# Kernel tuning notes

Hardware: AMD Instinct MI355X
Metric: run time of the kernel (lower is better)

The kernel has to match this reference:

```python
import jax, jax.numpy as jnp
import numpy as np

# Multi-res hash grid config (tiny-cuda-nn defaults matching input_ch=32 = 16 levels * 2 feats)
L = 16            # n_levels
F = 2             # n_features_per_level
T = 2 ** 19       # hashmap size per level
BASE_RES = 16
FINEST_RES = 512
_b = np.exp((np.log(FINEST_RES) - np.log(BASE_RES)) / (L - 1))
RES = np.floor(BASE_RES * (_b ** np.arange(L))).astype(np.float32)  # (L,)
PRIMES = jnp.array([1, 2654435761, 805459861], dtype=jnp.uint32)
# 8 binary corner offsets of a voxel
CORNERS = jnp.array([[(i >> d) & 1 for d in range(3)] for i in range(8)], dtype=jnp.uint32)  # (8,3)


def hash_encode(x, tables):
    """x: (N,3) in [0,1]; tables: (L, T, F). Returns (N, L*F)."""
    res = jnp.asarray(RES)                              # (L,)
    xs = x[None, :, :] * res[:, None, None]             # (L,N,3) scaled coords
    x0f = jnp.floor(xs)
    frac = xs - x0f                                     # (L,N,3)
    x0 = x0f.astype(jnp.uint32)
    corners = x0[:, :, None, :] + CORNERS[None, None]   # (L,N,8,3) uint32
    # spatial hash: xor of coord*prime, wraparound uint32 mul
    h = (corners[..., 0] * PRIMES[0]) ^ (corners[..., 1] * PRIMES[1]) ^ (corners[..., 2] * PRIMES[2])
    idx = (h % jnp.uint32(T)).astype(jnp.int32)         # (L,N,8)
    gidx = idx + (jnp.arange(L, dtype=jnp.int32) * T)[:, None, None]
    feats = tables.reshape(L * T, F)[gidx]              # (L,N,8,F) gather
    # trilinear weights per corner
    w = jnp.prod(jnp.where(CORNERS[None, None] == 1, frac[:, :, None, :], 1.0 - frac[:, :, None, :]), axis=-1)  # (L,N,8)
    out = jnp.einsum('lnc,lncf->lnf', w, feats)         # (L,N,F)
    return out.transpose(1, 0, 2).reshape(x.shape[0], L * F)


def setup_inputs() -> dict:
    key = jax.random.key(0)
    ks = jax.random.split(key, 16)
    N = 1048576
    W = 128
    pos_flat = jax.random.uniform(ks[0], (N, 3), dtype=jnp.float32)  # world pts in unit cube
    bbox_min = jnp.zeros((3,), dtype=jnp.float32)
    bbox_max = jnp.ones((3,), dtype=jnp.float32)
    tables = jax.random.uniform(ks[1], (L, T, F), dtype=jnp.float32, minval=-1e-4, maxval=1e-4)
    def lin(k, fan_in, fan_out):
        s = 1.0 / np.sqrt(fan_in)
        return jax.random.uniform(k, (fan_in, fan_out), dtype=jnp.float32, minval=-s, maxval=s)
    return {
        'pos_flat': pos_flat, 'bbox_min': bbox_min, 'bbox_max': bbox_max, 'tables': tables,
        'W0': lin(ks[2], L * F, W), 'b0': jnp.zeros((W,), jnp.float32),
        'W1': lin(ks[3], W, W), 'b1': jnp.zeros((W,), jnp.float32),
        'W2': lin(ks[4], W, W), 'b2': jnp.zeros((W,), jnp.float32),
        'W3': lin(ks[5], W, W), 'b3': jnp.zeros((W,), jnp.float32),
        'Wout': lin(ks[6], W, 4), 'bout': jnp.zeros((4,), jnp.float32),
    }


def reference(pos_flat, bbox_min, bbox_max, tables, W0, b0, W1, b1, W2, b2, W3, b3, Wout, bout):
    # normalize into canonical bbox [0,1]^3
    x = (pos_flat - bbox_min) / (bbox_max - bbox_min)
    h = hash_encode(x, tables)                # (N, 32)
    h = jax.nn.relu(h @ W0 + b0)
    h = jax.nn.relu(h @ W1 + b1)
    h = jax.nn.relu(h @ W2 + b2)
    h = jax.nn.relu(h @ W3 + b3)
    raws = h @ Wout + bout                    # (N, 4) rgb + density
    return raws
```

## Files before the change

kernel.cpp:

```cpp
#include <hip/hip_runtime.h>

typedef _Float16 half8 __attribute__((ext_vector_type(8)));
typedef _Float16 half4 __attribute__((ext_vector_type(4)));
typedef _Float16 half2 __attribute__((ext_vector_type(2)));
typedef float    f32x4 __attribute__((ext_vector_type(4)));
typedef float    f32x2 __attribute__((ext_vector_type(2)));
typedef unsigned u32x2 __attribute__((ext_vector_type(2)));
typedef unsigned u32x4 __attribute__((ext_vector_type(4)));

#define TMASK ((1u << 19) - 1u)
#define HSTRIDE 136
constexpr float SCALE = 65536.0f;
constexpr float INV_SCALE = 1.0f / 65536.0f;

__device__ __constant__ unsigned SC_TAB[8]   = {18, 22, 27, 34, 42, 52, 66, 82};
__device__ __constant__ unsigned SX4_TAB[8]  = {5, 6, 7, 9, 11, 13, 17, 21};
__device__ __constant__ unsigned DOFF16_TAB[8] = {0, 1620, 4524, 9627, 20031, 39435, 74587, 148639};
#define DSLOT_TOTAL 289843u

__global__ void prep_kernel(const float* __restrict__ W0, const float* __restrict__ W1,
                            const float* __restrict__ W2, const float* __restrict__ W3,
                            const float* __restrict__ Wm,
                            const float* __restrict__ b0, const float* __restrict__ b1,
                            const float* __restrict__ b2, const float* __restrict__ b3,
                            const float* __restrict__ bm,
                            _Float16* __restrict__ wsW, float* __restrict__ wsB,
                            const float* __restrict__ tabSrc, _Float16* __restrict__ tabF,
                            int tabBlocks)
{
    if ((int)blockIdx.x < tabBlocks) {
        size_t i = (size_t)blockIdx.x * 256 + threadIdx.x;
        f32x4 v = ((const f32x4*)tabSrc)[i];
        half4 o;
        o[0] = (_Float16)(v.x * SCALE);
        o[1] = (_Float16)(v.y * SCALE);
        o[2] = (_Float16)(v.z * SCALE);
        o[3] = (_Float16)(v.w * SCALE);
        ((half4*)tabF)[i] = o;
        return;
    }
    int gid = ((int)blockIdx.x - tabBlocks) * 256 + threadIdx.x;
    if (gid < 6912) {
        int tile = gid >> 6, lane = gid & 63;
        const float* W; int K, N, toff;
        if (tile < 8)        { W = W0; K = 32;  N = 128; toff = 0;   }
        else if (tile < 40)  { W = W1; K = 128; N = 128; toff = 8;   }
        else if (tile < 72)  { W = W2; K = 128; N = 128; toff = 40;  }
        else if (tile < 104) { W = W3; K = 128; N = 128; toff = 72;  }
        else                 { W = Wm; K = 128; N = 4;   toff = 104; }
        int tt = tile - toff;
        int KT = K >> 5;
        int nt = tt / KT, kt = tt - nt * KT;
        int n = nt * 16 + (lane & 15);
        int kbase = kt * 32 + (lane >> 4) * 8;
        half8 v;
        #pragma unroll
        for (int j = 0; j < 8; j++) {
            int k = kbase + j;
            float w = (n < N) ? W[k * N + n] : 0.0f;
            v[j] = (_Float16)w;
        }
        *(half8*)(wsW + (size_t)gid * 8) = v;
    } else if (gid < 6912 + 528) {
        int i = gid - 6912;
        float v;
        if (i < 512) {
            int layer = i >> 7, n = i & 127;
            const float* b = (layer == 0) ? b0 : (layer == 1) ? b1 : (layer == 2) ? b2 : b3;
            v = b[n] * SCALE;
        } else {
            int n = i - 512;
            v = (n < 4) ? bm[n] * SCALE : 0.0f;
        }
        wsB[i] = v;
    }
}

__global__ void dense_build(const float* __restrict__ tables, unsigned* __restrict__ dense)
{
    unsigned e = blockIdx.x * 256 + threadIdx.x;
    if (e >= DSLOT_TOTAL * 4u) return;
    unsigned slot = e >> 2, j = e & 3u;
    int l = 0;
    #pragma unroll
    for (int i = 1; i < 8; i++) l += (slot >= DOFF16_TAB[i]) ? 1 : 0;
    unsigned local = slot - DOFF16_TAB[l];
    unsigned s = SC_TAB[l], sx4 = SX4_TAB[l];
    unsigned plane = sx4 * s;
    unsigned z = local / plane;
    unsigned rem = local - z * plane;
    unsigned y = rem / sx4;
    unsigned xs = rem - y * sx4;
    unsigned x = xs * 4u + j;
    unsigned h = (x ^ (y * 2654435761u) ^ (z * 805459861u)) & TMASK;
    const float* src = tables + ((size_t)l * 524288u + h) * 2;
    half2 o; o[0] = (_Float16)(src[0] * SCALE); o[1] = (_Float16)(src[1] * SCALE);
    union { half2 h2; unsigned u; } cv; cv.h2 = o;
    dense[e] = cv.u;
}

struct PtState {
    unsigned fI0[4], fI1[4], cBase[4];
    unsigned kC;
    bool nx3f, nx3c;
    float fF[3], fC[3];
};
struct PtLoads {
    u32x4 fB[4]; u32x4 cS[4]; unsigned fX[4], cN[4];
};

__global__ __launch_bounds__(256) void encode_kernel(
    const float* __restrict__ pos, const float* __restrict__ bmn, const float* __restrict__ bmx,
    const _Float16* __restrict__ tabFine, const u32x4* __restrict__ dense16,
    _Float16* __restrict__ feat, int npts)
{
    const int lvl0 = (int)(blockIdx.x & 7);
    const int t = (int)threadIdx.x;
    const long pb = (long)(blockIdx.x >> 3) * 2048 + t;
    const float bx = bmn[0], by = bmn[1], bz = bmn[2];
    const float dxr = bmx[0] - bx, dyr = bmx[1] - by, dzr = bmx[2] - bz;
    constexpr float RESL[16] = {16.f, 20.f, 25.f, 32.f, 40.f, 50.f, 64.f, 80.f,
                                101.f, 128.f, 161.f, 203.f, 256.f, 322.f, 406.f, 512.f};
    const int l1 = lvl0 + 8;
    const _Float16* tblB = tabFine + ((size_t)lvl0 << 20);
    const float resF = RESL[l1], resC = RESL[lvl0];
    const unsigned sx4 = SX4_TAB[lvl0];
    const unsigned plane = sx4 * SC_TAB[lvl0];
    const u32x4* dptr = dense16 + DOFF16_TAB[lvl0];

    auto computePt = [&](long p, PtState& S) {
        const float nx = (pos[p * 3 + 0] - bx) / dxr;
        const float ny = (pos[p * 3 + 1] - by) / dyr;
        const float nz = (pos[p * 3 + 2] - bz) / dzr;
        {
            float xs = nx * resF, ys = ny * resF, zs = nz * resF;
            float fx = floorf(xs), fy = floorf(ys), fz = floorf(zs);
            unsigned xi = (unsigned)fx, yi = (unsigned)fy, zi = (unsigned)fz;
            S.fF[0] = xs - fx; S.fF[1] = ys - fy; S.fF[2] = zs - fz;
            unsigned hy0 = yi * 2654435761u, hy1 = (yi + 1u) * 2654435761u;
            unsigned hz0 = zi * 805459861u,  hz1 = (zi + 1u) * 805459861u;
            unsigned hyz[4] = {hy0 ^ hz0, hy1 ^ hz0, hy0 ^ hz1, hy1 ^ hz1};
            #pragma unroll
            for (int g = 0; g < 4; g++) {
                S.fI0[g] = (xi ^ hyz[g]) & TMASK;
                S.fI1[g] = ((xi + 1u) ^ hyz[g]) & TMASK;
            }
            S.nx3f = ((xi & 3u) == 3u);
        }
        {
            float xs = nx * resC, ys = ny * resC, zs = nz * resC;
            float fx = floorf(xs), fy = floorf(ys), fz = floorf(zs);
            unsigned xi = (unsigned)fx, yi = (unsigned)fy, zi = (unsigned)fz;
            S.fC[0] = xs - fx; S.fC[1] = ys - fy; S.fC[2] = zs - fz;
            unsigned b00 = (xi >> 2) + sx4 * yi + plane * zi;
            S.cBase[0] = b00;
            S.cBase[1] = b00 + sx4;
            S.cBase[2] = b00 + plane;
            S.cBase[3] = b00 + plane + sx4;
            S.kC = xi & 3u;
            S.nx3c = (S.kC == 3u);
        }
    };

    auto issuePt = [&](const PtState& S, PtLoads& L) {
        #pragma unroll
        for (int g = 0; g < 4; g++)
            L.fB[g] = *(const u32x4*)(tblB + (size_t)(S.fI0[g] >> 2) * 8);
        #pragma unroll
        for (int g = 0; g < 4; g++)
            L.cS[g] = dptr[S.cBase[g]];
        if (S.nx3f) {
            #pragma unroll
            for (int g = 0; g < 4; g++)
                L.fX[g] = *(const unsigned*)(tblB + (size_t)S.fI1[g] * 2);
        }
        if (S.nx3c) {
            #pragma unroll
            for (int g = 0; g < 4; g++)
                L.cN[g] = *(const unsigned*)(dptr + S.cBase[g] + 1);
        }
    };

    auto consumePt = [&](const PtState& S, const PtLoads& L, long p) {
        {
            float tx = S.fF[0], ty = S.fF[1], tz = S.fF[2];
            float wyz[4] = {(1.0f - ty) * (1.0f - tz), ty * (1.0f - tz),
                            (1.0f - ty) * tz,          ty * tz};
            float b0 = 0.0f, b1 = 0.0f;
            #pragma unroll
            for (int g = 0; g < 4; g++) {
                u32x4 v = L.fB[g];
                unsigned s0 = S.fI0[g] & 3u, s1 = S.fI1[g] & 3u;
                unsigned a0_ = (s0 & 2u) ? v[2] : v[0];
                unsigned b0_ = (s0 & 2u) ? v[3] : v[1];
                unsigned e0  = (s0 & 1u) ? b0_ : a0_;
                unsigned a1_ = (s1 & 2u) ? v[2] : v[0];
                unsigned b1_ = (s1 & 2u) ? v[3] : v[1];
                unsigned e1s = (s1 & 1u) ? b1_ : a1_;
                unsigned e1  = S.nx3f ? L.fX[g] : e1s;
                union { unsigned u; half2 h; } u0, u1;
                u0.u = e0; u1.u = e1;
                float w0 = wyz[g] * (1.0f - tx), w1 = wyz[g] * tx;
                b0 += w0 * (float)u0.h[0] + w1 * (float)u1.h[0];
                b1 += w0 * (float)u0.h[1] + w1 * (float)u1.h[1];
            }
            half2 ov2; ov2[0] = (_Float16)b0; ov2[1] = (_Float16)b1;
            union { half2 h; unsigned u; } cv; cv.h = ov2;
            __builtin_nontemporal_store(cv.u, (unsigned*)(feat + ((size_t)l1 * npts + p) * 2));
        }
        {
            float tx = S.fC[0], ty = S.fC[1], tz = S.fC[2];
            float wyz[4] = {(1.0f - ty) * (1.0f - tz), ty * (1.0f - tz),
                            (1.0f - ty) * tz,          ty * tz};
            unsigned k = S.kC;
            unsigned kp1 = (k < 3u) ? (k + 1u) : 0u;
            float a0 = 0.0f, a1 = 0.0f;
            #pragma unroll
            for (int g = 0; g < 4; g++) {
                union { unsigned u; half2 h; } u0, u1;
                u0.u = L.cS[g][k];
                u1.u = S.nx3c ? L.cN[g] : L.cS[g][kp1];
                float w0 = wyz[g] * (1.0f - tx), w1 = wyz[g] * tx;
                a0 += w0 * (float)u0.h[0] + w1 * (float)u1.h[0];
                a1 += w0 * (float)u0.h[1] + w1 * (float)u1.h[1];
            }
            half2 ov2; ov2[0] = (_Float16)a0; ov2[1] = (_Float16)a1;
            union { half2 h; unsigned u; } cv; cv.h = ov2;
            __builtin_nontemporal_store(cv.u, (unsigned*)(feat + ((size_t)lvl0 * npts + p) * 2));
        }
    };

    PtState sA, sB; PtLoads lA, lB;
    computePt(pb + 0 * 256, sA); issuePt(sA, lA);
    computePt(pb + 1 * 256, sB); issuePt(sB, lB);
    #pragma unroll
    for (int k = 0; k < 6; k++) {
        if ((k & 1) == 0) {
            consumePt(sA, lA, pb + (long)k * 256);
            computePt(pb + (long)(k + 2) * 256, sA); issuePt(sA, lA);
        } else {
            consumePt(sB, lB, pb + (long)k * 256);
            computePt(pb + (long)(k + 2) * 256, sB); issuePt(sB, lB);
        }
    }
    consumePt(sA, lA, pb + 6 * 256);
    consumePt(sB, lB, pb + 7 * 256);
}

#define ELANE 68

template<int KT, int TOFF>
__device__ __forceinline__ void layer_fwd4(half8 b[4][4], const half8* __restrict__ wf,
                                           const float* __restrict__ wsB, int li,
                                           unsigned* __restrict__ eb, int lane, int quad,
                                           unsigned srcA, unsigned srcB, int mtbase)
{
    unsigned* wptr = eb + lane * ELANE;
    #pragma unroll
    for (int mt = 0; mt < 8; mt++) {
        f32x4 bias = *(const f32x4*)&wsB[li * 128 + mt * 16 + quad * 4];
        half8 w[KT];
        #pragma unroll
        for (int kt = 0; kt < KT; kt++)
            w[kt] = wf[(size_t)(TOFF + mt * KT + kt) * 64 + lane];
        f32x4 acc[4] = {bias, bias, bias, bias};
        #pragma unroll
        for (int nt = 0; nt < 4; nt++)
            #pragma unroll
            for (int kt = 0; kt < KT; kt++)
                acc[nt] = __builtin_amdgcn_mfma_f32_16x16x32_f16(w[kt], b[nt][kt], acc[nt], 0, 0, 0);
        #pragma unroll
        for (int np = 0; np < 2; np++) {
            union { _Float16 h[8]; u32x4 v; } pk;
            #pragma unroll
            for (int r = 0; r < 4; r++) {
                pk.h[r]     = (_Float16)fmaxf(acc[2 * np][r],     0.0f);
                pk.h[4 + r] = (_Float16)fmaxf(acc[2 * np + 1][r], 0.0f);
            }
            *(u32x4*)(wptr + mt * 8 + np * 4) = pk.v;
        }
    }
    #pragma unroll
    for (int ktp = 0; ktp < 4; ktp++) {
        int mt = 2 * ktp + mtbase;
        u32x4 rA0 = *(const u32x4*)(eb + srcA * ELANE + mt * 8);
        u32x4 rA1 = *(const u32x4*)(eb + srcA * ELANE + mt * 8 + 4);
        u32x4 rB0 = *(const u32x4*)(eb + srcB * ELANE + mt * 8);
        u32x4 rB1 = *(const u32x4*)(eb + srcB * ELANE + mt * 8 + 4);
        union { u32x4 v; half8 h; } c0, c1, c2, c3;
        c0.v = (u32x4){rA0[0], rA0[1], rB0[0], rB0[1]};
        c1.v = (u32x4){rA0[2], rA0[3], rB0[2], rB0[3]};
        c2.v = (u32x4){rA1[0], rA1[1], rB1[0], rB1[1]};
        c3.v = (u32x4){rA1[2], rA1[3], rB1[2], rB1[3]};
        b[0][ktp] = c0.h;
        b[1][ktp] = c1.h;
        b[2][ktp] = c2.h;
        b[3][ktp] = c3.h;
    }
}

__global__ __launch_bounds__(256) void mlp_kernel(
    const unsigned* __restrict__ feat32, const half8* __restrict__ wf,
    const float* __restrict__ wsB, float* __restrict__ out, int npts)
{
    __shared__ __align__(16) unsigned ebuf[4 * 64 * ELANE];
    const int t = threadIdx.x;
    const int lane = t & 63, wv = t >> 6;
    const int col = lane & 15, quad = lane >> 4;
    const long base = (long)blockIdx.x * 256 + wv * 64;
    unsigned* eb = ebuf + wv * (64 * ELANE);
    const int q1 = 2 * (quad & 1);
    const unsigned srcA = (unsigned)(col + 16 * q1);
    const unsigned srcB = (unsigned)(col + 16 * (q1 + 1));
    const int mtbase = quad >> 1;

    half8 b[4][4];
    #pragma unroll
    for (int nt = 0; nt < 4; nt++) {
        const long pt = base + nt * 16 + col;
        union { unsigned u4[4]; half8 v; } cv;
        #pragma unroll
        for (int jj = 0; jj < 4; jj++)
            cv.u4[jj] = feat32[(size_t)(quad * 4 + jj) * npts + pt];
        b[nt][0] = cv.v;
    }

    layer_fwd4<1, 0 >(b, wf, wsB, 0, eb, lane, quad, srcA, srcB, mtbase);
    layer_fwd4<4, 8 >(b, wf, wsB, 1, eb, lane, quad, srcA, srcB, mtbase);
    layer_fwd4<4, 40>(b, wf, wsB, 2, eb, lane, quad, srcA, srcB, mtbase);
    layer_fwd4<4, 72>(b, wf, wsB, 3, eb, lane, quad, srcA, srcB, mtbase);

    f32x4 biaso = *(const f32x4*)&wsB[512 + quad * 4];
    f32x4 acco[4] = {biaso, biaso, biaso, biaso};
    #pragma unroll
    for (int kt = 0; kt < 4; kt++) {
        half8 w = wf[(size_t)(104 + kt) * 64 + lane];
        #pragma unroll
        for (int nt = 0; nt < 4; nt++)
            acco[nt] = __builtin_amdgcn_mfma_f32_16x16x32_f16(w, b[nt][kt], acco[nt], 0, 0, 0);
    }
    if (quad == 0) {
        #pragma unroll
        for (int nt = 0; nt < 4; nt++) {
            f32x4 v;
            #pragma unroll
            for (int r = 0; r < 4; r++) v[r] = acco[nt][r] * INV_SCALE;
            *(f32x4*)(out + (base + nt * 16 + col) * 4) = v;
        }
    }
}

template<int KT, int TOFF, bool RELU>
__device__ __forceinline__ void mlp_layer(_Float16* h, const half8* __restrict__ wf,
                                          const float* __restrict__ wsB, int layerIdx,
                                          int m0, int lane)
{
    const int col = lane & 15, quad = lane >> 4;
    const int sw = (col & 3) << 3;
    half8 a[2][KT];
    #pragma unroll
    for (int mt = 0; mt < 2; mt++)
        #pragma unroll
        for (int kt = 0; kt < KT; kt++)
            a[mt][kt] = *(const half8*)&h[(m0 + mt * 16 + col) * HSTRIDE + ((kt * 32 + quad * 8) ^ sw)];
    f32x4 acc[2][8];
    #pragma unroll
    for (int nt = 0; nt < 8; nt++) {
        float bv = wsB[layerIdx * 128 + nt * 16 + col];
        acc[0][nt] = (f32x4){bv, bv, bv, bv};
        acc[1][nt] = (f32x4){bv, bv, bv, bv};
    }
    #pragma unroll
    for (int nt = 0; nt < 8; nt++) {
        half8 b[KT];
        #pragma unroll
        for (int kt = 0; kt < KT; kt++)
            b[kt] = wf[(size_t)(TOFF + nt * KT + kt) * 64 + lane];
        #pragma unroll
        for (int mt = 0; mt < 2; mt++)
            #pragma unroll
            for (int kt = 0; kt < KT; kt++)
                acc[mt][nt] = __builtin_amdgcn_mfma_f32_16x16x32_f16(a[mt][kt], b[kt], acc[mt][nt], 0, 0, 0);
    }
    #pragma unroll
    for (int mt = 0; mt < 2; mt++)
        #pragma unroll
        for (int nt = 0; nt < 8; nt++) {
            f32x4 v = acc[mt][nt];
            #pragma unroll
            for (int r = 0; r < 4; r++) {
                float x = v[r];
                if (RELU) x = fmaxf(x, 0.0f);
                h[(m0 + mt * 16 + quad * 4 + r) * HSTRIDE + ((nt * 16 + col) ^ (r << 3))] = (_Float16)x;
            }
        }
}

__global__ __launch_bounds__(256, 2) void fused_kernel(
    const float* __restrict__ pos, const float* __restrict__ bmn, const float* __restrict__ bmx,
    const float* __restrict__ tables, const half8* __restrict__ wf, const float* __restrict__ wsB,
    float* __restrict__ out)
{
    __shared__ _Float16 hbuf[128 * HSTRIDE];
    __shared__ float outstage[512];
    const int t = threadIdx.x;
    const long base = (long)blockIdx.x * 128;
    {
        const int p = t >> 1, hh = t & 1;
        const long gp = base + p;
        const float b0x = bmn[0], b0y = bmn[1], b0z = bmn[2];
        const float nx = (pos[gp * 3 + 0] - b0x) / (bmx[0] - b0x);
        const float ny = (pos[gp * 3 + 1] - b0y) / (bmx[1] - b0y);
        const float nz = (pos[gp * 3 + 2] - b0z) / (bmx[2] - b0z);
        constexpr float RLO[8] = {16.f, 20.f, 25.f, 32.f, 40.f, 50.f, 64.f, 80.f};
        constexpr float RHI[8] = {101.f, 128.f, 161.f, 203.f, 256.f, 322.f, 406.f, 512.f};
        half8 fa, fb;
        #pragma unroll
        for (int li = 0; li < 8; li++) {
            const float res = hh ? RHI[li] : RLO[li];
            const float* tbl = tables + ((size_t)(hh * 8 + li) << 20);
            float xs = nx * res, ys = ny * res, zs = nz * res;
            float fx = floorf(xs), fy = floorf(ys), fz = floorf(zs);
            unsigned xi = (unsigned)fx, yi = (unsigned)fy, zi = (unsigned)fz;
            float tx = xs - fx, ty = ys - fy, tz = zs - fz;
            unsigned hx[2] = {xi, xi + 1u};
            unsigned hy[2] = {yi * 2654435761u, (yi + 1u) * 2654435761u};
            unsigned hz[2] = {zi * 805459861u, (zi + 1u) * 805459861u};
            float wx[2] = {1.0f - tx, tx}, wy[2] = {1.0f - ty, ty}, wz[2] = {1.0f - tz, tz};
            float a0 = 0.0f, a1 = 0.0f;
            #pragma unroll
            for (int c = 0; c < 8; c++) {
                unsigned hsh = hx[c & 1] ^ hy[(c >> 1) & 1] ^ hz[c >> 2];
                unsigned idx = hsh & TMASK;
                f32x2 f = *(const f32x2*)(tbl + (size_t)idx * 2);
                float w = wx[c & 1] * wy[(c >> 1) & 1] * wz[c >> 2];
                a0 += w * f.x;
                a1 += w * f.y;
            }
            if (li < 4) { fa[2 * li]       = (_Float16)(a0 * SCALE); fa[2 * li + 1]       = (_Float16)(a1 * SCALE); }
            else        { fb[2 * (li - 4)] = (_Float16)(a0 * SCALE); fb[2 * (li - 4) + 1] = (_Float16)(a1 * SCALE); }
        }
        const int sw = (p & 3) << 3;
        *(half8*)&hbuf[p * HSTRIDE + ((hh * 16) ^ sw)]       = fa;
        *(half8*)&hbuf[p * HSTRIDE + (((hh * 16) + 8) ^ sw)] = fb;
    }
    __syncthreads();
    {
        const int lane = t & 63;
        const int m0 = (t >> 6) * 32;
        mlp_layer<1, 0,   true>(hbuf, wf, wsB, 0, m0, lane);
        mlp_layer<4, 8,   true>(hbuf, wf, wsB, 1, m0, lane);
        mlp_layer<4, 40,  true>(hbuf, wf, wsB, 2, m0, lane);
        mlp_layer<4, 72,  true>(hbuf, wf, wsB, 3, m0, lane);
        const int col = lane & 15, quad = lane >> 4;
        const int sw = (col & 3) << 3;
        half8 a[2][4];
        #pragma unroll
        for (int mt = 0; mt < 2; mt++)
            #pragma unroll
            for (int kt = 0; kt < 4; kt++)
                a[mt][kt] = *(const half8*)&hbuf[(m0 + mt * 16 + col) * HSTRIDE + ((kt * 32 + quad * 8) ^ sw)];
        float bv = wsB[512 + col];
        f32x4 acc[2] = {(f32x4){bv, bv, bv, bv}, (f32x4){bv, bv, bv, bv}};
        #pragma unroll
        for (int kt = 0; kt < 4; kt++) {
            half8 bfr = wf[(size_t)(104 + kt) * 64 + lane];
            #pragma unroll
            for (int mt = 0; mt < 2; mt++)
                acc[mt] = __builtin_amdgcn_mfma_f32_16x16x32_f16(a[mt][kt], bfr, acc[mt], 0, 0, 0);
        }
        if (col < 4) {
            #pragma unroll
            for (int mt = 0; mt < 2; mt++)
                #pragma unroll
                for (int r = 0; r < 4; r++)
                    outstage[(m0 + mt * 16 + quad * 4 + r) * 4 + col] = acc[mt][r] * INV_SCALE;
        }
    }
    __syncthreads();
    if (t < 128) {
        f32x4 v = ((const f32x4*)outstage)[t];
        *(f32x4*)(out + (base + t) * 4) = v;
    }
}

extern "C" void kernel_launch(void* const* d_in, const int* in_sizes, int n_in,
                              void* d_out, int out_size, void* d_ws, size_t ws_size,
                              hipStream_t stream) {
    const float* pos    = (const float*)d_in[0];
    const float* bmn    = (const float*)d_in[1];
    const float* bmx    = (const float*)d_in[2];
    const float* tables = (const float*)d_in[3];
    const float* W0 = (const float*)d_in[4];
    const float* b0 = (const float*)d_in[5];
    const float* W1 = (const float*)d_in[6];
    const float* b1 = (const float*)d_in[7];
    const float* W2 = (const float*)d_in[8];
    const float* b2 = (const float*)d_in[9];
    const float* W3 = (const float*)d_in[10];
    const float* b3 = (const float*)d_in[11];
    const float* Wm = (const float*)d_in[12];
    const float* bm = (const float*)d_in[13];

    const int N = in_sizes[0] / 3;
    const size_t featBytes    = (size_t)N * 16 * 4;
    const size_t tabFineBytes = (size_t)8 * 524288 * 2 * 2;
    const size_t denseBytes   = ((size_t)DSLOT_TOTAL * 16 + 255) & ~(size_t)255;
    const size_t need = featBytes + tabFineBytes + denseBytes + 110592 + 2112;

    if (ws_size >= need && (N % 2048) == 0) {
        _Float16* feat  = (_Float16*)d_ws;
        _Float16* tabF  = (_Float16*)((char*)d_ws + featBytes);
        unsigned* dense = (unsigned*)((char*)d_ws + featBytes + tabFineBytes);
        _Float16* wsW   = (_Float16*)((char*)d_ws + featBytes + tabFineBytes + denseBytes);
        float*    wsB   = (float*)((char*)d_ws + featBytes + tabFineBytes + denseBytes + 110592);
        prep_kernel<<<8192 + 30, 256, 0, stream>>>(W0, W1, W2, W3, Wm, b0, b1, b2, b3, bm,
                                                   wsW, wsB, tables + (size_t)8 * 524288 * 2,
                                                   tabF, 8192);
        dense_build<<<(DSLOT_TOTAL * 4 + 255) / 256, 256, 0, stream>>>(tables, dense);
        encode_kernel<<<(N / 2048) * 8, 256, 0, stream>>>(pos, bmn, bmx, tabF,
                                                          (const u32x4*)dense, feat, N);
        mlp_kernel<<<N / 256, 256, 0, stream>>>((const unsigned*)feat, (const half8*)wsW,
                                                wsB, (float*)d_out, N);
    } else {
        _Float16* wsW = (_Float16*)d_ws;
        float*    wsB = (float*)((char*)d_ws + 110592);
        prep_kernel<<<30, 256, 0, stream>>>(W0, W1, W2, W3, Wm, b0, b1, b2, b3, bm,
                                            wsW, wsB, tables, (_Float16*)nullptr, 0);
        fused_kernel<<<N / 128, 256, 0, stream>>>(pos, bmn, bmx, tables,
                                                  (const half8*)wsW, wsB, (float*)d_out);
    }
}
```

Before: 585.6 us.

## Store coarse-level dense grids as 4x2 x-y bricks to halve gathers

Rebuilds the dense coarse-level tables as bricks of 4 x-cells by 2 y-rows, 32 bytes per slot, so each z-slice of a voxel's corners is fetched with one 16-byte load. That cuts the coarse-level gathers from four loads plus up to four boundary loads down to two. The fine-level path now packs its selection bits into one word and derives the x+1 index with an XOR, which trims register use. The cost is a dense buffer twice as large, more work in the build kernel, and 16-byte loads that are only 8-byte aligned. The old slot layout is kept as a fallback when the workspace is too small.

```diff
diff --git a/kernel.cpp b/kernel.cpp
--- a/kernel.cpp
+++ b/kernel.cpp
@@ -76,7 +76,31 @@
     }
 }
 
-__global__ void dense_build(const float* __restrict__ tables, unsigned* __restrict__ dense)
+__global__ void dense_build_brick(const float* __restrict__ tables, unsigned* __restrict__ dense)
+{
+    unsigned e = blockIdx.x * 256 + threadIdx.x;
+    if (e >= DSLOT_TOTAL * 8u) return;
+    unsigned brick = e >> 3, j = e & 7u;
+    int l = 0;
+    #pragma unroll
+    for (int i = 1; i < 8; i++) l += (brick >= DOFF16_TAB[i]) ? 1 : 0;
+    unsigned local = brick - DOFF16_TAB[l];
+    unsigned s = SC_TAB[l], sx4 = SX4_TAB[l];
+    unsigned plane = sx4 * s;
+    unsigned z = local / plane;
+    unsigned rem = local - z * plane;
+    unsigned yb = rem / sx4;
+    unsigned xs = rem - yb * sx4;
+    unsigned x = xs * 4u + (j >> 1);
+    unsigned y = yb + (j & 1u);
+    unsigned h = (x ^ (y * 2654435761u) ^ (z * 805459861u)) & TMASK;
+    const float* src = tables + ((size_t)l * 524288u + h) * 2;
+    half2 o; o[0] = (_Float16)(src[0] * SCALE); o[1] = (_Float16)(src[1] * SCALE);
+    union { half2 h2; unsigned u; } cv; cv.h2 = o;
+    dense[e] = cv.u;
+}
+
+__global__ void dense_build_slot(const float* __restrict__ tables, unsigned* __restrict__ dense)
 {
     unsigned e = blockIdx.x * 256 + threadIdx.x;
     if (e >= DSLOT_TOTAL * 4u) return;
@@ -99,17 +123,163 @@
     dense[e] = cv.u;
 }
 
-struct PtState {
+struct PtStateB {
+    unsigned fI0[4];
+    unsigned xm1, fSel;
+    unsigned cOff0, cOff1;
+    float fF[3], fC[3];
+};
+struct PtLoadsB {
+    u32x4 fB[4]; u32x4 cZ[2]; unsigned fX[4];
+};
+
+__global__ __launch_bounds__(256) void encode_brick(
+    const float* __restrict__ pos, const float* __restrict__ bmn, const float* __restrict__ bmx,
+    const _Float16* __restrict__ tabFine, const unsigned* __restrict__ dense,
+    _Float16* __restrict__ feat, int npts)
+{
+    const int lvl0 = (int)(blockIdx.x & 7);
+    const int t = (int)threadIdx.x;
+    const long pb = (long)(blockIdx.x >> 3) * 2048 + t;
+    const float bx = bmn[0], by = bmn[1], bz = bmn[2];
+    const float dxr = bmx[0] - bx, dyr = bmx[1] - by, dzr = bmx[2] - bz;
+    constexpr float RESL[16] = {16.f, 20.f, 25.f, 32.f, 40.f, 50.f, 64.f, 80.f,
+                                101.f, 128.f, 161.f, 203.f, 256.f, 322.f, 406.f, 512.f};
+    const int l1 = lvl0 + 8;
+    const _Float16* tblB = tabFine + ((size_t)lvl0 << 20);
+    const float resF = RESL[l1], resC = RESL[lvl0];
+    const unsigned sx4 = SX4_TAB[lvl0];
+    const unsigned plane8 = sx4 * SC_TAB[lvl0] * 8u;
+    const unsigned* dlvl = dense + (size_t)DOFF16_TAB[lvl0] * 8u;
+
+    auto computePt = [&](long p, PtStateB& S) {
+        const float nx = (pos[p * 3 + 0] - bx) / dxr;
+        const float ny = (pos[p * 3 + 1] - by) / dyr;
+        const float nz = (pos[p * 3 + 2] - bz) / dzr;
+        {
+            float xs = nx * resF, ys = ny * resF, zs = nz * resF;
+            float fx = floorf(xs), fy = floorf(ys), fz = floorf(zs);
+            unsigned xi = (unsigned)fx, yi = (unsigned)fy, zi = (unsigned)fz;
+            S.fF[0] = xs - fx; S.fF[1] = ys - fy; S.fF[2] = zs - fz;
+            unsigned hy0 = yi * 2654435761u, hy1 = (yi + 1u) * 2654435761u;
+            unsigned hz0 = zi * 805459861u,  hz1 = (zi + 1u) * 805459861u;
+            unsigned hyz[4] = {hy0 ^ hz0, hy1 ^ hz0, hy0 ^ hz1, hy1 ^ hz1};
+            unsigned xm1 = xi ^ (xi + 1u);
+            unsigned sel = 0;
+            #pragma unroll
+            for (int g = 0; g < 4; g++) {
+                unsigned i0 = (xi ^ hyz[g]) & TMASK;
+                S.fI0[g] = i0;
+                sel |= (i0 & 3u) << (2 * g);
+            }
+            sel |= (xm1 & 3u) << 8;
+            if ((xi & 3u) == 3u) sel |= 1024u;
+            S.fSel = sel;
+            S.xm1 = xm1;
+        }
+        {
+            float xs = nx * resC, ys = ny * resC, zs = nz * resC;
+            float fx = floorf(xs), fy = floorf(ys), fz = floorf(zs);
+            unsigned xi = (unsigned)fx, yi = (unsigned)fy, zi = (unsigned)fz;
+            S.fC[0] = xs - fx; S.fC[1] = ys - fy; S.fC[2] = zs - fz;
+            unsigned o0 = ((xi >> 2) + sx4 * yi) * 8u + plane8 * zi + (xi & 3u) * 2u;
+            S.cOff0 = o0;
+            S.cOff1 = o0 + plane8;
+        }
+    };
+
+    auto issuePt = [&](const PtStateB& S, PtLoadsB& L) {
+        #pragma unroll
+        for (int g = 0; g < 4; g++)
+            L.fB[g] = *(const u32x4*)(tblB + (size_t)(S.fI0[g] >> 2) * 8);
+        __builtin_memcpy(&L.cZ[0], dlvl + S.cOff0, 16);
+        __builtin_memcpy(&L.cZ[1], dlvl + S.cOff1, 16);
+        if (S.fSel & 1024u) {
+            #pragma unroll
+            for (int g = 0; g < 4; g++)
+                L.fX[g] = *(const unsigned*)(tblB + (size_t)((S.fI0[g] ^ S.xm1) & TMASK) * 2);
+        }
+    };
+
+    auto consumePt = [&](const PtStateB& S, const PtLoadsB& L, long p) {
+        {
+            float tx = S.fF[0], ty = S.fF[1], tz = S.fF[2];
+            float wyz[4] = {(1.0f - ty) * (1.0f - tz), ty * (1.0f - tz),
+                            (1.0f - ty) * tz,          ty * tz};
+            unsigned selw = S.fSel;
+            unsigned m = (selw >> 8) & 3u;
+            bool carry = (selw & 1024u) != 0u;
+            float b0 = 0.0f, b1 = 0.0f;
+            #pragma unroll
+            for (int g = 0; g < 4; g++) {
+                u32x4 v = L.fB[g];
+                unsigned s0 = (selw >> (2 * g)) & 3u;
+                unsigned s1 = s0 ^ m;
+                unsigned a0_ = (s0 & 2u) ? v[2] : v[0];
+                unsigned b0_ = (s0 & 2u) ? v[3] : v[1];
+                unsigned e0  = (s0 & 1u) ? b0_ : a0_;
+                unsigned a1_ = (s1 & 2u) ? v[2] : v[0];
+                unsigned b1_ = (s1 & 2u) ? v[3] : v[1];
+                unsigned e1s = (s1 & 1u) ? b1_ : a1_;
+                unsigned e1  = carry ? L.fX[g] : e1s;
+                union { unsigned u; half2 h; } u0, u1;
+                u0.u = e0; u1.u = e1;
+                float w0 = wyz[g] * (1.0f - tx), w1 = wyz[g] * tx;
+                b0 += w0 * (float)u0.h[0] + w1 * (float)u1.h[0];
+                b1 += w0 * (float)u0.h[1] + w1 * (float)u1.h[1];
+            }
+            half2 ov2; ov2[0] = (_Float16)b0; ov2[1] = (_Float16)b1;
+            union { half2 h; unsigned u; } cv; cv.h = ov2;
+            __builtin_nontemporal_store(cv.u, (unsigned*)(feat + ((size_t)l1 * npts + p) * 2));
+        }
+        {
+            float tx = S.fC[0], ty = S.fC[1], tz = S.fC[2];
+            float wyz[4] = {(1.0f - ty) * (1.0f - tz), ty * (1.0f - tz),
+                            (1.0f - ty) * tz,          ty * tz};
+            float a0 = 0.0f, a1 = 0.0f;
+            #pragma unroll
+            for (int g = 0; g < 4; g++) {
+                union { unsigned u; half2 h; } u0, u1;
+                u0.u = L.cZ[g >> 1][g & 1];
+                u1.u = L.cZ[g >> 1][2 + (g & 1)];
+                float w0 = wyz[g] * (1.0f - tx), w1 = wyz[g] * tx;
+                a0 += w0 * (float)u0.h[0] + w1 * (float)u1.h[0];
+                a1 += w0 * (float)u0.h[1] + w1 * (float)u1.h[1];
+            }
+            half2 ov2; ov2[0] = (_Float16)a0; ov2[1] = (_Float16)a1;
+            union { half2 h; unsigned u; } cv; cv.h = ov2;
+            __builtin_nontemporal_store(cv.u, (unsigned*)(feat + ((size_t)lvl0 * npts + p) * 2));
+        }
+    };
+
+    PtStateB sA, sB; PtLoadsB lA, lB;
+    computePt(pb + 0 * 256, sA); issuePt(sA, lA);
+    computePt(pb + 1 * 256, sB); issuePt(sB, lB);
+    #pragma unroll
+    for (int k = 0; k < 6; k++) {
+        if ((k & 1) == 0) {
+            consumePt(sA, lA, pb + (long)k * 256);
+            computePt(pb + (long)(k + 2) * 256, sA); issuePt(sA, lA);
+        } else {
+            consumePt(sB, lB, pb + (long)k * 256);
+            computePt(pb + (long)(k + 2) * 256, sB); issuePt(sB, lB);
+        }
+    }
+    consumePt(sA, lA, pb + 6 * 256);
+    consumePt(sB, lB, pb + 7 * 256);
+}
+
+struct PtStateS {
     unsigned fI0[4], fI1[4], cBase[4];
     unsigned kC;
     bool nx3f, nx3c;
     float fF[3], fC[3];
 };
-struct PtLoads {
+struct PtLoadsS {
     u32x4 fB[4]; u32x4 cS[4]; unsigned fX[4], cN[4];
 };
 
-__global__ __launch_bounds__(256) void encode_kernel(
+__global__ __launch_bounds__(256) void encode_slot(
     const float* __restrict__ pos, const float* __restrict__ bmn, const float* __restrict__ bmx,
     const _Float16* __restrict__ tabFine, const u32x4* __restrict__ dense16,
     _Float16* __restrict__ feat, int npts)
@@ -128,7 +298,7 @@
     const unsigned plane = sx4 * SC_TAB[lvl0];
     const u32x4* dptr = dense16 + DOFF16_TAB[lvl0];
 
-    auto computePt = [&](long p, PtState& S) {
+    auto computePt = [&](long p, PtStateS& S) {
         const float nx = (pos[p * 3 + 0] - bx) / dxr;
         const float ny = (pos[p * 3 + 1] - by) / dyr;
         const float nz = (pos[p * 3 + 2] - bz) / dzr;
@@ -162,7 +332,7 @@
         }
     };
 
-    auto issuePt = [&](const PtState& S, PtLoads& L) {
+    auto issuePt = [&](const PtStateS& S, PtLoadsS& L) {
         #pragma unroll
         for (int g = 0; g < 4; g++)
             L.fB[g] = *(const u32x4*)(tblB + (size_t)(S.fI0[g] >> 2) * 8);
@@ -181,7 +351,7 @@
         }
     };
 
-    auto consumePt = [&](const PtState& S, const PtLoads& L, long p) {
+    auto consumePt = [&](const PtStateS& S, const PtLoadsS& L, long p) {
         {
             float tx = S.fF[0], ty = S.fF[1], tz = S.fF[2];
             float wyz[4] = {(1.0f - ty) * (1.0f - tz), ty * (1.0f - tz),
@@ -230,7 +400,7 @@
         }
     };
 
-    PtState sA, sB; PtLoads lA, lB;
+    PtStateS sA, sB; PtLoadsS lA, lB;
     computePt(pb + 0 * 256, sA); issuePt(sA, lA);
     computePt(pb + 1 * 256, sB); issuePt(sB, lB);
     #pragma unroll
@@ -505,21 +675,37 @@
     const int N = in_sizes[0] / 3;
     const size_t featBytes    = (size_t)N * 16 * 4;
     const size_t tabFineBytes = (size_t)8 * 524288 * 2 * 2;
-    const size_t denseBytes   = ((size_t)DSLOT_TOTAL * 16 + 255) & ~(size_t)255;
-    const size_t need = featBytes + tabFineBytes + denseBytes + 110592 + 2112;
-
-    if (ws_size >= need && (N % 2048) == 0) {
+    const size_t denseBytesB  = ((size_t)DSLOT_TOTAL * 32 + 255) & ~(size_t)255;
+    const size_t denseBytesS  = ((size_t)DSLOT_TOTAL * 16 + 255) & ~(size_t)255;
+    const size_t needB = featBytes + tabFineBytes + denseBytesB + 110592 + 2112;
+    const size_t needS = featBytes + tabFineBytes + denseBytesS + 110592 + 2112;
+
+    if (ws_size >= needB && (N % 2048) == 0) {
         _Float16* feat  = (_Float16*)d_ws;
         _Float16* tabF  = (_Float16*)((char*)d_ws + featBytes);
         unsigned* dense = (unsigned*)((char*)d_ws + featBytes + tabFineBytes);
-        _Float16* wsW   = (_Float16*)((char*)d_ws + featBytes + tabFineBytes + denseBytes);
-        float*    wsB   = (float*)((char*)d_ws + featBytes + tabFineBytes + denseBytes + 110592);
+        _Float16* wsW   = (_Float16*)((char*)d_ws + featBytes + tabFineBytes + denseBytesB);
+        float*    wsB   = (float*)((char*)d_ws + featBytes + tabFineBytes + denseBytesB + 110592);
         prep_kernel<<<8192 + 30, 256, 0, stream>>>(W0, W1, W2, W3, Wm, b0, b1, b2, b3, bm,
                                                    wsW, wsB, tables + (size_t)8 * 524288 * 2,
                                                    tabF, 8192);
-        dense_build<<<(DSLOT_TOTAL * 4 + 255) / 256, 256, 0, stream>>>(tables, dense);
-        encode_kernel<<<(N / 2048) * 8, 256, 0, stream>>>(pos, bmn, bmx, tabF,
-                                                          (const u32x4*)dense, feat, N);
+        dense_build_brick<<<(DSLOT_TOTAL * 8 + 255) / 256, 256, 0, stream>>>(tables, dense);
+        encode_brick<<<(N / 2048) * 8, 256, 0, stream>>>(pos, bmn, bmx, tabF,
+                                                         dense, feat, N);
+        mlp_kernel<<<N / 256, 256, 0, stream>>>((const unsigned*)feat, (const half8*)wsW,
+                                                wsB, (float*)d_out, N);
+    } else if (ws_size >= needS && (N % 2048) == 0) {
+        _Float16* feat  = (_Float16*)d_ws;
+        _Float16* tabF  = (_Float16*)((char*)d_ws + featBytes);
+        unsigned* dense = (unsigned*)((char*)d_ws + featBytes + tabFineBytes);
+        _Float16* wsW   = (_Float16*)((char*)d_ws + featBytes + tabFineBytes + denseBytesS);
+        float*    wsB   = (float*)((char*)d_ws + featBytes + tabFineBytes + denseBytesS + 110592);
+        prep_kernel<<<8192 + 30, 256, 0, stream>>>(W0, W1, W2, W3, Wm, b0, b1, b2, b3, bm,
+                                                   wsW, wsB, tables + (size_t)8 * 524288 * 2,
+                                                   tabF, 8192);
+        dense_build_slot<<<(DSLOT_TOTAL * 4 + 255) / 256, 256, 0, stream>>>(tables, dense);
+        encode_slot<<<(N / 2048) * 8, 256, 0, stream>>>(pos, bmn, bmx, tabF,
+                                                        (const u32x4*)dense, feat, N);
         mlp_kernel<<<N / 256, 256, 0, stream>>>((const unsigned*)feat, (const half8*)wsW,
                                                 wsB, (float*)d_out, N);
     } else {
```

Result: faster. 520.8 us (-11.1%).

## Use y-paired brick layout for coarse dense grid and merge prep kernels

Applied to the files above, without the earlier changes.

Replaces the coarse-level dense table with bricks that interleave x and y+1 neighbours, so each point reads two 16-byte loads (z and z+1) instead of four slot loads plus conditional neighbour loads. The x+1 cell is read from the same brick at an offset. The weight/table prep and dense build are fused into one launch, and the fine and coarse features of a level pair are written together as one 8-byte store, with the MLP's feature read indexing changed to match. The cost is a dense buffer twice as large, possibly unaligned 16-byte loads via memcpy, and a larger combined prep kernel.

```diff
diff --git a/kernel.cpp b/kernel.cpp
--- a/kernel.cpp
+++ b/kernel.cpp
@@ -17,6 +17,88 @@
 __device__ __constant__ unsigned SX4_TAB[8]  = {5, 6, 7, 9, 11, 13, 17, 21};
 __device__ __constant__ unsigned DOFF16_TAB[8] = {0, 1620, 4524, 9627, 20031, 39435, 74587, 148639};
 #define DSLOT_TOTAL 289843u
+
+__global__ void prep_dense_kernel(const float* __restrict__ W0, const float* __restrict__ W1,
+                                  const float* __restrict__ W2, const float* __restrict__ W3,
+                                  const float* __restrict__ Wm,
+                                  const float* __restrict__ b0, const float* __restrict__ b1,
+                                  const float* __restrict__ b2, const float* __restrict__ b3,
+                                  const float* __restrict__ bm,
+                                  _Float16* __restrict__ wsW, float* __restrict__ wsB,
+                                  const float* __restrict__ tables, _Float16* __restrict__ tabF,
+                                  unsigned* __restrict__ dense)
+{
+    const int bid = (int)blockIdx.x;
+    if (bid < 8192) {
+        size_t i = (size_t)bid * 256 + threadIdx.x;
+        f32x4 v = ((const f32x4*)(tables + (size_t)8 * 524288 * 2))[i];
+        half4 o;
+        o[0] = (_Float16)(v.x * SCALE);
+        o[1] = (_Float16)(v.y * SCALE);
+        o[2] = (_Float16)(v.z * SCALE);
+        o[3] = (_Float16)(v.w * SCALE);
+        ((half4*)tabF)[i] = o;
+        return;
+    }
+    if (bid < 8222) {
+        int gid = (bid - 8192) * 256 + threadIdx.x;
+        if (gid < 6912) {
+            int tile = gid >> 6, lane = gid & 63;
+            const float* W; int K, N, toff;
+            if (tile < 8)        { W = W0; K = 32;  N = 128; toff = 0;   }
+            else if (tile < 40)  { W = W1; K = 128; N = 128; toff = 8;   }
+            else if (tile < 72)  { W = W2; K = 128; N = 128; toff = 40;  }
+            else if (tile < 104) { W = W3; K = 128; N = 128; toff = 72;  }
+            else                 { W = Wm; K = 128; N = 4;   toff = 104; }
+            int tt = tile - toff;
+            int KT = K >> 5;
+            int nt = tt / KT, kt = tt - nt * KT;
+            int n = nt * 16 + (lane & 15);
+            int kbase = kt * 32 + (lane >> 4) * 8;
+            half8 v;
+            #pragma unroll
+            for (int j = 0; j < 8; j++) {
+                int k = kbase + j;
+                float w = (n < N) ? W[k * N + n] : 0.0f;
+                v[j] = (_Float16)w;
+            }
+            *(half8*)(wsW + (size_t)gid * 8) = v;
+        } else if (gid < 6912 + 528) {
+            int i = gid - 6912;
+            float v;
+            if (i < 512) {
+                int layer = i >> 7, n = i & 127;
+                const float* b = (layer == 0) ? b0 : (layer == 1) ? b1 : (layer == 2) ? b2 : b3;
+                v = b[n] * SCALE;
+            } else {
+                int n = i - 512;
+                v = (n < 4) ? bm[n] * SCALE : 0.0f;
+            }
+            wsB[i] = v;
+        }
+        return;
+    }
+    unsigned e = (unsigned)(bid - 8222) * 256 + threadIdx.x;
+    if (e >= DSLOT_TOTAL * 8u) return;
+    unsigned brick = e >> 3, j = e & 7u;
+    int l = 0;
+    #pragma unroll
+    for (int i = 1; i < 8; i++) l += (brick >= DOFF16_TAB[i]) ? 1 : 0;
+    unsigned local = brick - DOFF16_TAB[l];
+    unsigned s = SC_TAB[l], sx4 = SX4_TAB[l];
+    unsigned plane = sx4 * s;
+    unsigned z = local / plane;
+    unsigned rem = local - z * plane;
+    unsigned yb = rem / sx4;
+    unsigned xs = rem - yb * sx4;
+    unsigned x = xs * 4u + (j >> 1);
+    unsigned y = yb + (j & 1u);
+    unsigned h = (x ^ (y * 2654435761u) ^ (z * 805459861u)) & TMASK;
+    const float* src = tables + ((size_t)l * 524288u + h) * 2;
+    half2 o; o[0] = (_Float16)(src[0] * SCALE); o[1] = (_Float16)(src[1] * SCALE);
+    union { half2 h2; unsigned u; } cv; cv.h2 = o;
+    dense[e] = cv.u;
+}
 
 __global__ void prep_kernel(const float* __restrict__ W0, const float* __restrict__ W1,
                             const float* __restrict__ W2, const float* __restrict__ W3,
@@ -76,42 +158,19 @@
     }
 }
 
-__global__ void dense_build(const float* __restrict__ tables, unsigned* __restrict__ dense)
-{
-    unsigned e = blockIdx.x * 256 + threadIdx.x;
-    if (e >= DSLOT_TOTAL * 4u) return;
-    unsigned slot = e >> 2, j = e & 3u;
-    int l = 0;
-    #pragma unroll
-    for (int i = 1; i < 8; i++) l += (slot >= DOFF16_TAB[i]) ? 1 : 0;
-    unsigned local = slot - DOFF16_TAB[l];
-    unsigned s = SC_TAB[l], sx4 = SX4_TAB[l];
-    unsigned plane = sx4 * s;
-    unsigned z = local / plane;
-    unsigned rem = local - z * plane;
-    unsigned y = rem / sx4;
-    unsigned xs = rem - y * sx4;
-    unsigned x = xs * 4u + j;
-    unsigned h = (x ^ (y * 2654435761u) ^ (z * 805459861u)) & TMASK;
-    const float* src = tables + ((size_t)l * 524288u + h) * 2;
-    half2 o; o[0] = (_Float16)(src[0] * SCALE); o[1] = (_Float16)(src[1] * SCALE);
-    union { half2 h2; unsigned u; } cv; cv.h2 = o;
-    dense[e] = cv.u;
-}
-
-struct PtState {
-    unsigned fI0[4], fI1[4], cBase[4];
-    unsigned kC;
-    bool nx3f, nx3c;
+struct PtStateB {
+    unsigned fI0[4];
+    unsigned xm1, fSel;
+    unsigned cOff0, cOff1;
     float fF[3], fC[3];
 };
-struct PtLoads {
-    u32x4 fB[4]; u32x4 cS[4]; unsigned fX[4], cN[4];
+struct PtLoadsB {
+    u32x4 fB[4]; u32x4 cZ[2]; unsigned fX[4];
 };
 
-__global__ __launch_bounds__(256) void encode_kernel(
+__global__ __launch_bounds__(256) void encode_brick(
     const float* __restrict__ pos, const float* __restrict__ bmn, const float* __restrict__ bmx,
-    const _Float16* __restrict__ tabFine, const u32x4* __restrict__ dense16,
+    const _Float16* __restrict__ tabFine, const unsigned* __restrict__ dense,
     _Float16* __restrict__ feat, int npts)
 {
     const int lvl0 = (int)(blockIdx.x & 7);
@@ -125,10 +184,10 @@
     const _Float16* tblB = tabFine + ((size_t)lvl0 << 20);
     const float resF = RESL[l1], resC = RESL[lvl0];
     const unsigned sx4 = SX4_TAB[lvl0];
-    const unsigned plane = sx4 * SC_TAB[lvl0];
-    const u32x4* dptr = dense16 + DOFF16_TAB[lvl0];
-
-    auto computePt = [&](long p, PtState& S) {
+    const unsigned plane8 = sx4 * SC_TAB[lvl0] * 8u;
+    const unsigned* dlvl = dense + (size_t)DOFF16_TAB[lvl0] * 8u;
+
+    auto computePt = [&](long p, PtStateB& S) {
         const float nx = (pos[p * 3 + 0] - bx) / dxr;
         const float ny = (pos[p * 3 + 1] - by) / dyr;
         const float nz = (pos[p * 3 + 2] - bz) / dzr;
@@ -140,64 +199,65 @@
             unsigned hy0 = yi * 2654435761u, hy1 = (yi + 1u) * 2654435761u;
             unsigned hz0 = zi * 805459861u,  hz1 = (zi + 1u) * 805459861u;
             unsigned hyz[4] = {hy0 ^ hz0, hy1 ^ hz0, hy0 ^ hz1, hy1 ^ hz1};
+            unsigned xm1 = xi ^ (xi + 1u);
+            unsigned sel = 0;
             #pragma unroll
             for (int g = 0; g < 4; g++) {
-                S.fI0[g] = (xi ^ hyz[g]) & TMASK;
-                S.fI1[g] = ((xi + 1u) ^ hyz[g]) & TMASK;
-            }
-            S.nx3f = ((xi & 3u) == 3u);
+                unsigned i0 = (xi ^ hyz[g]) & TMASK;
+                S.fI0[g] = i0;
+                sel |= (i0 & 3u) << (2 * g);
+            }
+            sel |= (xm1 & 3u) << 8;
+            if ((xi & 3u) == 3u) sel |= 1024u;
+            S.fSel = sel;
+            S.xm1 = xm1;
         }
         {
             float xs = nx * resC, ys = ny * resC, zs = nz * resC;
             float fx = floorf(xs), fy = floorf(ys), fz = floorf(zs);
             unsigned xi = (unsigned)fx, yi = (unsigned)fy, zi = (unsigned)fz;
             S.fC[0] = xs - fx; S.fC[1] = ys - fy; S.fC[2] = zs - fz;
-            unsigned b00 = (xi >> 2) + sx4 * yi + plane * zi;
-            S.cBase[0] = b00;
-            S.cBase[1] = b00 + sx4;
-            S.cBase[2] = b00 + plane;
-            S.cBase[3] = b00 + plane + sx4;
-            S.kC = xi & 3u;
-            S.nx3c = (S.kC == 3u);
+            unsigned o0 = ((xi >> 2) + sx4 * yi) * 8u + plane8 * zi + (xi & 3u) * 2u;
+            S.cOff0 = o0;
+            S.cOff1 = o0 + plane8;
         }
     };
 
-    auto issuePt = [&](const PtState& S, PtLoads& L) {
+    auto issuePt = [&](const PtStateB& S, PtLoadsB& L) {
         #pragma unroll
         for (int g = 0; g < 4; g++)
             L.fB[g] = *(const u32x4*)(tblB + (size_t)(S.fI0[g] >> 2) * 8);
-        #pragma unroll
-        for (int g = 0; g < 4; g++)
-            L.cS[g] = dptr[S.cBase[g]];
-        if (S.nx3f) {
+        __builtin_memcpy(&L.cZ[0], dlvl + S.cOff0, 16);
+        __builtin_memcpy(&L.cZ[1], dlvl + S.cOff1, 16);
+        if (S.fSel & 1024u) {
             #pragma unroll
             for (int g = 0; g < 4; g++)
-                L.fX[g] = *(const unsigned*)(tblB + (size_t)S.fI1[g] * 2);
-        }
-        if (S.nx3c) {
-            #pragma unroll
-            for (int g = 0; g < 4; g++)
-                L.cN[g] = *(const unsigned*)(dptr + S.cBase[g] + 1);
+                L.fX[g] = *(const unsigned*)(tblB + (size_t)((S.fI0[g] ^ S.xm1) & TMASK) * 2);
         }
     };
 
-    auto consumePt = [&](const PtState& S, const PtLoads& L, long p) {
+    auto consumePt = [&](const PtStateB& S, const PtLoadsB& L, long p) {
+        unsigned fineU, coarseU;
         {
             float tx = S.fF[0], ty = S.fF[1], tz = S.fF[2];
             float wyz[4] = {(1.0f - ty) * (1.0f - tz), ty * (1.0f - tz),
                             (1.0f - ty) * tz,          ty * tz};
+            unsigned selw = S.fSel;
+            unsigned m = (selw >> 8) & 3u;
+            bool carry = (selw & 1024u) != 0u;
             float b0 = 0.0f, b1 = 0.0f;
             #pragma unroll
             for (int g = 0; g < 4; g++) {
                 u32x4 v = L.fB[g];
-                unsigned s0 = S.fI0[g] & 3u, s1 = S.fI1[g] & 3u;
+                unsigned s0 = (selw >> (2 * g)) & 3u;
+                unsigned s1 = s0 ^ m;
                 unsigned a0_ = (s0 & 2u) ? v[2] : v[0];
                 unsigned b0_ = (s0 & 2u) ? v[3] : v[1];
                 unsigned e0  = (s0 & 1u) ? b0_ : a0_;
                 unsigned a1_ = (s1 & 2u) ? v[2] : v[0];
                 unsigned b1_ = (s1 & 2u) ? v[3] : v[1];
                 unsigned e1s = (s1 & 1u) ? b1_ : a1_;
-                unsigned e1  = S.nx3f ? L.fX[g] : e1s;
+                unsigned e1  = carry ? L.fX[g] : e1s;
                 union { unsigned u; half2 h; } u0, u1;
                 u0.u = e0; u1.u = e1;
                 float w0 = wyz[g] * (1.0f - tx), w1 = wyz[g] * tx;
@@ -206,31 +266,31 @@
             }
             half2 ov2; ov2[0] = (_Float16)b0; ov2[1] = (_Float16)b1;
             union { half2 h; unsigned u; } cv; cv.h = ov2;
-            __builtin_nontemporal_store(cv.u, (unsigned*)(feat + ((size_t)l1 * npts + p) * 2));
+            fineU = cv.u;
         }
         {
             float tx = S.fC[0], ty = S.fC[1], tz = S.fC[2];
             float wyz[4] = {(1.0f - ty) * (1.0f - tz), ty * (1.0f - tz),
                             (1.0f - ty) * tz,          ty * tz};
-            unsigned k = S.kC;
-            unsigned kp1 = (k < 3u) ? (k + 1u) : 0u;
             float a0 = 0.0f, a1 = 0.0f;
             #pragma unroll
             for (int g = 0; g < 4; g++) {
                 union { unsigned u; half2 h; } u0, u1;
-                u0.u = L.cS[g][k];
-                u1.u = S.nx3c ? L.cN[g] : L.cS[g][kp1];
+                u0.u = L.cZ[g >> 1][g & 1];
+                u1.u = L.cZ[g >> 1][2 + (g & 1)];
                 float w0 = wyz[g] * (1.0f - tx), w1 = wyz[g] * tx;
                 a0 += w0 * (float)u0.h[0] + w1 * (float)u1.h[0];
                 a1 += w0 * (float)u0.h[1] + w1 * (float)u1.h[1];
             }
             half2 ov2; ov2[0] = (_Float16)a0; ov2[1] = (_Float16)a1;
             union { half2 h; unsigned u; } cv; cv.h = ov2;
-            __builtin_nontemporal_store(cv.u, (unsigned*)(feat + ((size_t)lvl0 * npts + p) * 2));
-        }
+            coarseU = cv.u;
+        }
+        u32x2 sv; sv[0] = coarseU; sv[1] = fineU;
+        __builtin_nontemporal_store(sv, (u32x2*)(feat + ((size_t)lvl0 * npts + p) * 4));
     };
 
-    PtState sA, sB; PtLoads lA, lB;
+    PtStateB sA, sB; PtLoadsB lA, lB;
     computePt(pb + 0 * 256, sA); issuePt(sA, lA);
     computePt(pb + 1 * 256, sB); issuePt(sB, lB);
     #pragma unroll
@@ -313,6 +373,8 @@
     const unsigned srcA = (unsigned)(col + 16 * q1);
     const unsigned srcB = (unsigned)(col + 16 * (q1 + 1));
     const int mtbase = quad >> 1;
+    const int pibase = (quad & 1) * 4;
+    const int comp = quad >> 1;
 
     half8 b[4][4];
     #pragma unroll
@@ -321,7 +383,7 @@
         union { unsigned u4[4]; half8 v; } cv;
         #pragma unroll
         for (int jj = 0; jj < 4; jj++)
-            cv.u4[jj] = feat32[(size_t)(quad * 4 + jj) * npts + pt];
+            cv.u4[jj] = feat32[((size_t)(pibase + jj) * npts + pt) * 2 + comp];
         b[nt][0] = cv.v;
     }
 
@@ -505,21 +567,19 @@
     const int N = in_sizes[0] / 3;
     const size_t featBytes    = (size_t)N * 16 * 4;
     const size_t tabFineBytes = (size_t)8 * 524288 * 2 * 2;
-    const size_t denseBytes   = ((size_t)DSLOT_TOTAL * 16 + 255) & ~(size_t)255;
-    const size_t need = featBytes + tabFineBytes + denseBytes + 110592 + 2112;
-
-    if (ws_size >= need && (N % 2048) == 0) {
+    const size_t denseBytesB  = ((size_t)DSLOT_TOTAL * 32 + 255) & ~(size_t)255;
+    const size_t needB = featBytes + tabFineBytes + denseBytesB + 110592 + 2112;
+
+    if (ws_size >= needB && (N % 2048) == 0) {
         _Float16* feat  = (_Float16*)d_ws;
         _Float16* tabF  = (_Float16*)((char*)d_ws + featBytes);
         unsigned* dense = (unsigned*)((char*)d_ws + featBytes + tabFineBytes);
-        _Float16* wsW   = (_Float16*)((char*)d_ws + featBytes + tabFineBytes + denseBytes);
-        float*    wsB   = (float*)((char*)d_ws + featBytes + tabFineBytes + denseBytes + 110592);
-        prep_kernel<<<8192 + 30, 256, 0, stream>>>(W0, W1, W2, W3, Wm, b0, b1, b2, b3, bm,
-                                                   wsW, wsB, tables + (size_t)8 * 524288 * 2,
-                                                   tabF, 8192);
-        dense_build<<<(DSLOT_TOTAL * 4 + 255) / 256, 256, 0, stream>>>(tables, dense);
-        encode_kernel<<<(N / 2048) * 8, 256, 0, stream>>>(pos, bmn, bmx, tabF,
-                                                          (const u32x4*)dense, feat, N);
+        _Float16* wsW   = (_Float16*)((char*)d_ws + featBytes + tabFineBytes + denseBytesB);
+        float*    wsB   = (float*)((char*)d_ws + featBytes + tabFineBytes + denseBytesB + 110592);
+        prep_dense_kernel<<<8192 + 30 + (DSLOT_TOTAL * 8 + 255) / 256, 256, 0, stream>>>(
+            W0, W1, W2, W3, Wm, b0, b1, b2, b3, bm, wsW, wsB, tables, tabF, dense);
+        encode_brick<<<(N / 2048) * 8, 256, 0, stream>>>(pos, bmn, bmx, tabF,
+                                                         dense, feat, N);
         mlp_kernel<<<N / 256, 256, 0, stream>>>((const unsigned*)feat, (const half8*)wsW,
                                                 wsB, (float*)d_out, N);
     } else {
```

Measured after the change: 517.3 us. 1.13x faster.
